# Kernel tuning notes

Hardware: AMD Instinct MI355X
Metric: run time of the kernel (lower is better)

## Reference

```python
import jax, jax.numpy as jnp
import numpy as np

B, T, Z, S, H = 32, 128, 100, 6, 64
F1, F2 = 512, 128


def setup_inputs() -> dict:
    key = jax.random.key(0)
    ks = jax.random.split(key, 11)
    g = lambda k, shape, sc: (jax.random.normal(k, shape, dtype=jnp.float32) * sc)
    return {
        "x": jax.random.normal(ks[0], (B, T, Z, S), dtype=jnp.float32),
        "W_ih": g(ks[1], (3 * H, S), 0.125),   # GRU input weights [r|z|n]
        "W_hh": g(ks[2], (3 * H, H), 0.125),   # GRU hidden weights [r|z|n]
        "b_ih": g(ks[3], (3 * H,), 0.125),
        "b_hh": g(ks[4], (3 * H,), 0.125),
        "w1": g(ks[5], (F1, H), 0.1),
        "b1": g(ks[6], (F1,), 0.1),
        "w2": g(ks[7], (F2, F1), 0.04),
        "b2": g(ks[8], (F2,), 0.04),
        "w3": g(ks[9], (1, F2), 0.09),
        "b3": g(ks[10], (1,), 0.09),
    }


def reference(x, W_ih, W_hh, b_ih, b_hh, w1, b1, w2, b2, w3, b3):
    b, t, z, s = x.shape
    h_dim = W_hh.shape[1]
    # Fuse the per-zone python loop into the batch dim, zone-major so the
    # final reshape matches torch.stack(a).view(-1, t, nzones).
    xm = jnp.transpose(x, (2, 0, 1, 3)).reshape(z * b, t, s)  # (ZB, T, S)
    # Precompute input projections for all timesteps (one big GEMM).
    gi_all = jnp.einsum('nts,gs->ntg', xm, W_ih) + b_ih        # (ZB, T, 3H)

    def step(h, gi):
        gh = h @ W_hh.T + b_hh
        r = jax.nn.sigmoid(gi[:, :h_dim] + gh[:, :h_dim])
        zg = jax.nn.sigmoid(gi[:, h_dim:2 * h_dim] + gh[:, h_dim:2 * h_dim])
        n = jnp.tanh(gi[:, 2 * h_dim:] + r * gh[:, 2 * h_dim:])
        h_new = (1.0 - zg) * n + zg * h
        return h_new, h_new

    h0 = jnp.zeros((z * b, h_dim), x.dtype)
    _, sx = jax.lax.scan(step, h0, jnp.swapaxes(gi_all, 0, 1))  # (T, ZB, H)
    sx = jnp.swapaxes(sx, 0, 1)                                  # (ZB, T, H)

    a1 = jax.nn.relu(sx @ w1.T + b1)
    a2 = jax.nn.relu(a1 @ w2.T + b2)
    a3 = a2 @ w3.T + b3                                          # (ZB, T, 1)
    return a3.reshape(-1, t, z)                                  # (B, T, Z)
```

## Files before the change

### kernel.cpp

```cpp
#include <hip/hip_runtime.h>
#include <stdint.h>

#define Tdim 128
#define Zdim 100
#define Sdim 6
#define Hdim 64
#define ZB   3200
#define F1   512
#define F2   128
#define Mrows (ZB * Tdim)

typedef _Float16 f16x8 __attribute__((ext_vector_type(8)));
typedef _Float16 f16x4 __attribute__((ext_vector_type(4)));
typedef float f32x4 __attribute__((ext_vector_type(4)));
typedef uint32_t u32x4 __attribute__((ext_vector_type(4)));

__device__ __forceinline__ float sigmoidf_fast(float x) {
  return 1.f / (1.f + __expf(-x));
}
__device__ __forceinline__ float tanhf_fast(float x) {
  return 1.f - 2.f / (__expf(2.f * x) + 1.f);
}

__global__ __launch_bounds__(256) void prep_kernel(
    const float* __restrict__ W_ih, const float* __restrict__ W_hh,
    const float* __restrict__ w1, const float* __restrict__ w2,
    _Float16* __restrict__ Wf, _Float16* __restrict__ w1p,
    _Float16* __restrict__ w2p) {
  int i = blockIdx.x * 256 + threadIdx.x;
  if (i < 192 * 96) {
    int g = i / 96, k = i - g * 96;
    float v = (k < 64) ? W_hh[g * 64 + k] : ((k < 70) ? W_ih[g * 6 + (k - 64)] : 0.f);
    Wf[i] = (_Float16)v;
  }
  int j = i - 192 * 96;
  if (j >= 0 && j < 16 * 32 * 72) {
    int kt = j / 2304, r = j - kt * 2304;
    int f1 = r / 72, h = r - f1 * 72;
    w1p[j] = (_Float16)((h < 64) ? w1[(kt * 32 + f1) * 64 + h] : 0.f);
  }
  int l = j - 16 * 32 * 72;
  if (l >= 0 && l < 16 * 128 * 40) {
    int kt = l / 5120, r = l - kt * 5120;
    int f2 = r / 40, k = r - f2 * 40;
    w2p[l] = (_Float16)((k < 32) ? w2[f2 * 512 + kt * 32 + k] : 0.f);
  }
}

__global__ __launch_bounds__(256, 1) void gru_kernel(
    const float* __restrict__ x, const _Float16* __restrict__ Wf,
    const float* __restrict__ b_ih, const float* __restrict__ b_hh,
    _Float16* __restrict__ sx) {
  __shared__ __align__(16) _Float16 hist[32][16][72];
  __shared__ __align__(16) _Float16 xs[Tdim][16][8];
  const int tid = threadIdx.x;
  const int lane = tid & 63;
  const int w = tid >> 6;
  const int c = lane & 15;
  const int q = lane >> 4;

  for (int i = 0; i < 8; i++) {
    int idx = i * 256 + tid;
    int t = idx >> 4, row = idx & 15;
    int nr = blockIdx.x * 16 + row;
    const float* p = x + (size_t)(nr & 31) * (Tdim * Zdim * Sdim)
                       + (size_t)t * (Zdim * Sdim) + (size_t)(nr >> 5) * Sdim;
    f16x8 v;
    v[0] = (_Float16)p[0]; v[1] = (_Float16)p[1]; v[2] = (_Float16)p[2];
    v[3] = (_Float16)p[3]; v[4] = (_Float16)p[4]; v[5] = (_Float16)p[5];
    v[6] = (_Float16)0.f;  v[7] = (_Float16)0.f;
    *(f16x8*)&xs[t][row][0] = v;
  }

  const int gr0 = w * 16;
  const int gz0 = 64 + w * 16;
  const int gn0 = 128 + w * 16;

  f16x8 Ar[3], Az[3], Anh[2], Ani;
#pragma unroll
  for (int kf = 0; kf < 3; kf++) {
    Ar[kf] = *(const f16x8*)(Wf + (size_t)(gr0 + c) * 96 + kf * 32 + q * 8);
    Az[kf] = *(const f16x8*)(Wf + (size_t)(gz0 + c) * 96 + kf * 32 + q * 8);
  }
  Anh[0] = *(const f16x8*)(Wf + (size_t)(gn0 + c) * 96 + q * 8);
  Anh[1] = *(const f16x8*)(Wf + (size_t)(gn0 + c) * 96 + 32 + q * 8);
  Ani    = *(const f16x8*)(Wf + (size_t)(gn0 + c) * 96 + 64 + q * 8);

  f32x4 Cr, Cz, Cnh, Cni;
  {
    f32x4 bir = *(const f32x4*)(b_ih + gr0 + q * 4);
    f32x4 bhr = *(const f32x4*)(b_hh + gr0 + q * 4);
    f32x4 biz = *(const f32x4*)(b_ih + gz0 + q * 4);
    f32x4 bhz = *(const f32x4*)(b_hh + gz0 + q * 4);
#pragma unroll
    for (int r = 0; r < 4; r++) { Cr[r] = bir[r] + bhr[r]; Cz[r] = biz[r] + bhz[r]; }
    Cnh = *(const f32x4*)(b_hh + gn0 + q * 4);
    Cni = *(const f32x4*)(b_ih + gn0 + q * 4);
  }

  __syncthreads();

  f16x8 Bh0 = {0, 0, 0, 0, 0, 0, 0, 0};
  f16x8 Bh1 = {0, 0, 0, 0, 0, 0, 0, 0};
  f32x4 hprev = {0.f, 0.f, 0.f, 0.f};

  for (int t = 0; t < Tdim; t++) {
    const int tc = t & 31;
    f16x8 xv8 = *(const f16x8*)&xs[t][c][0];
    f16x8 Bx;
#pragma unroll
    for (int j = 0; j < 8; j++) Bx[j] = (q == 0) ? xv8[j] : (_Float16)0.f;

    f32x4 Dni = __builtin_amdgcn_mfma_f32_16x16x32_f16(Ani, Bx, Cni, 0, 0, 0);
    f32x4 Dr  = __builtin_amdgcn_mfma_f32_16x16x32_f16(Ar[2], Bx, Cr, 0, 0, 0);
    f32x4 Dz  = __builtin_amdgcn_mfma_f32_16x16x32_f16(Az[2], Bx, Cz, 0, 0, 0);
    f32x4 Dnh = __builtin_amdgcn_mfma_f32_16x16x32_f16(Anh[0], Bh0, Cnh, 0, 0, 0);
    Dr  = __builtin_amdgcn_mfma_f32_16x16x32_f16(Ar[0], Bh0, Dr, 0, 0, 0);
    Dz  = __builtin_amdgcn_mfma_f32_16x16x32_f16(Az[0], Bh0, Dz, 0, 0, 0);
    Dnh = __builtin_amdgcn_mfma_f32_16x16x32_f16(Anh[1], Bh1, Dnh, 0, 0, 0);
    Dr  = __builtin_amdgcn_mfma_f32_16x16x32_f16(Ar[1], Bh1, Dr, 0, 0, 0);
    Dz  = __builtin_amdgcn_mfma_f32_16x16x32_f16(Az[1], Bh1, Dz, 0, 0, 0);

    f16x4 pk;
#pragma unroll
    for (int r = 0; r < 4; r++) {
      float rr = sigmoidf_fast(Dr[r]);
      float zg = sigmoidf_fast(Dz[r]);
      float nn = tanhf_fast(Dni[r] + rr * Dnh[r]);
      float hnew = nn + zg * (hprev[r] - nn);
      hprev[r] = hnew;
      pk[r] = (_Float16)hnew;
    }
    *(f16x4*)&hist[tc][c][w * 16 + q * 4] = pk;
    __syncthreads();
    Bh0 = *(const f16x8*)&hist[tc][c][q * 8];
    Bh1 = *(const f16x8*)&hist[tc][c][32 + q * 8];

    if (tc == 31) {
      const int t0 = t - 31;
#pragma unroll
      for (int rr2 = 0; rr2 < 4; rr2++) {
        const int row = w * 4 + rr2;
        const int nrow = blockIdx.x * 16 + row;
        _Float16* dst = sx + (size_t)nrow * Tdim * Hdim + (size_t)t0 * Hdim;
#pragma unroll
        for (int it = 0; it < 4; it++) {
          int idx = it * 64 + lane;
          int tcc = idx >> 3, hd8 = idx & 7;
          f16x8 vv = *(const f16x8*)&hist[tcc][row][hd8 * 8];
          *(f16x8*)(dst + tcc * 64 + hd8 * 8) = vv;
        }
      }
      __syncthreads();
    }
  }
}

__global__ __launch_bounds__(256, 3) void mlp_kernel(
    const _Float16* __restrict__ sx, const _Float16* __restrict__ w1p,
    const _Float16* __restrict__ w2p, const float* __restrict__ b1,
    const float* __restrict__ b2, const float* __restrict__ w3,
    const float* __restrict__ b3, float* __restrict__ out) {
  __shared__ __align__(16) _Float16 w1s[2][32][72];
  __shared__ __align__(16) _Float16 w2s[2][128][40];
  __shared__ __align__(16) _Float16 rep[4][2][2][16][36];
  const int tid = threadIdx.x;
  const int lane = tid & 63;
  const int wave = tid >> 6;
  const int c = lane & 15;
  const int q = lane >> 4;
  const size_t m0 = ((size_t)blockIdx.x * 4 + wave) * 32;

  f16x8 Bs[2][2];
#pragma unroll
  for (int g = 0; g < 2; g++)
#pragma unroll
    for (int kk = 0; kk < 2; kk++)
      Bs[g][kk] = *(const f16x8*)(sx + (m0 + g * 16 + c) * Hdim + kk * 32 + q * 8);

  f32x4 acc2[2][8];
#pragma unroll
  for (int g = 0; g < 2; g++)
#pragma unroll
    for (int nt = 0; nt < 8; nt++) acc2[g][nt] = (f32x4){0.f, 0.f, 0.f, 0.f};

  u32x4 r1a, r1b, r2a, r2b, r2c;
  {
    const u32x4* g1 = (const u32x4*)(w1p);
    const u32x4* g2 = (const u32x4*)(w2p);
    r1a = g1[tid];
    if (tid < 32) r1b = g1[256 + tid];
    r2a = g2[tid];
    r2b = g2[256 + tid];
    if (tid < 128) r2c = g2[512 + tid];
    u32x4* s1 = (u32x4*)&w1s[0][0][0];
    u32x4* s2 = (u32x4*)&w2s[0][0][0];
    s1[tid] = r1a;
    if (tid < 32) s1[256 + tid] = r1b;
    s2[tid] = r2a;
    s2[256 + tid] = r2b;
    if (tid < 128) s2[512 + tid] = r2c;
  }
  __syncthreads();

#pragma unroll 2
  for (int kt = 0; kt < 16; kt++) {
    const int buf = kt & 1;
    if (kt + 1 < 16) {
      const u32x4* g1 = (const u32x4*)(w1p + (size_t)(kt + 1) * 2304);
      const u32x4* g2 = (const u32x4*)(w2p + (size_t)(kt + 1) * 5120);
      r1a = g1[tid];
      if (tid < 32) r1b = g1[256 + tid];
      r2a = g2[tid];
      r2b = g2[256 + tid];
      if (tid < 128) r2c = g2[512 + tid];
    }

#pragma unroll
    for (int ntl = 0; ntl < 2; ntl++) {
      const int f1b = kt * 32 + ntl * 16;
      f16x8 A0 = *(const f16x8*)&w1s[buf][ntl * 16 + c][q * 8];
      f16x8 A1 = *(const f16x8*)&w1s[buf][ntl * 16 + c][32 + q * 8];
      f32x4 bb = *(const f32x4*)(b1 + f1b + q * 4);
#pragma unroll
      for (int g = 0; g < 2; g++) {
        f32x4 cc = {0.f, 0.f, 0.f, 0.f};
        cc = __builtin_amdgcn_mfma_f32_16x16x32_f16(A0, Bs[g][0], cc, 0, 0, 0);
        cc = __builtin_amdgcn_mfma_f32_16x16x32_f16(A1, Bs[g][1], cc, 0, 0, 0);
        f16x4 pk;
#pragma unroll
        for (int r = 0; r < 4; r++) {
          float v = cc[r] + bb[r];
          pk[r] = (_Float16)(v > 0.f ? v : 0.f);
        }
        *(f16x4*)&rep[wave][buf][g][c][ntl * 16 + q * 4] = pk;
      }
    }
    f16x8 Ba[2];
#pragma unroll
    for (int g = 0; g < 2; g++) {
      f16x4 lo = *(const f16x4*)&rep[wave][buf][g][c][q * 8];
      f16x4 hi = *(const f16x4*)&rep[wave][buf][g][c][q * 8 + 4];
#pragma unroll
      for (int j = 0; j < 4; j++) { Ba[g][j] = lo[j]; Ba[g][4 + j] = hi[j]; }
    }
#pragma unroll
    for (int nt = 0; nt < 8; nt++) {
      f16x8 A2 = *(const f16x8*)&w2s[buf][nt * 16 + c][q * 8];
#pragma unroll
      for (int g = 0; g < 2; g++)
        acc2[g][nt] = __builtin_amdgcn_mfma_f32_16x16x32_f16(A2, Ba[g], acc2[g][nt], 0, 0, 0);
    }

    if (kt + 1 < 16) {
      u32x4* s1 = (u32x4*)&w1s[buf ^ 1][0][0];
      u32x4* s2 = (u32x4*)&w2s[buf ^ 1][0][0];
      s1[tid] = r1a;
      if (tid < 32) s1[256 + tid] = r1b;
      s2[tid] = r2a;
      s2[256 + tid] = r2b;
      if (tid < 128) s2[512 + tid] = r2c;
      __syncthreads();
    }
  }

  float part[2] = {0.f, 0.f};
#pragma unroll
  for (int nt = 0; nt < 8; nt++) {
    f32x4 bb = *(const f32x4*)(b2 + nt * 16 + q * 4);
    f32x4 ww = *(const f32x4*)(w3 + nt * 16 + q * 4);
#pragma unroll
    for (int g = 0; g < 2; g++) {
#pragma unroll
      for (int r = 0; r < 4; r++) {
        float v = acc2[g][nt][r] + bb[r];
        v = v > 0.f ? v : 0.f;
        part[g] = fmaf(v, ww[r], part[g]);
      }
    }
  }
#pragma unroll
  for (int g = 0; g < 2; g++) {
    part[g] += __shfl_xor(part[g], 16, 64);
    part[g] += __shfl_xor(part[g], 32, 64);
  }
  if (q < 2) {
    float pv = (q == 0) ? part[0] : part[1];
    out[m0 + q * 16 + c] = pv + b3[0];
  }
}

extern "C" void kernel_launch(void* const* d_in, const int* in_sizes, int n_in,
                              void* d_out, int out_size, void* d_ws, size_t ws_size,
                              hipStream_t stream) {
  const float* x    = (const float*)d_in[0];
  const float* W_ih = (const float*)d_in[1];
  const float* W_hh = (const float*)d_in[2];
  const float* b_ih = (const float*)d_in[3];
  const float* b_hh = (const float*)d_in[4];
  const float* w1   = (const float*)d_in[5];
  const float* b1   = (const float*)d_in[6];
  const float* w2   = (const float*)d_in[7];
  const float* b2   = (const float*)d_in[8];
  const float* w3   = (const float*)d_in[9];
  const float* b3   = (const float*)d_in[10];
  float* out = (float*)d_out;

  char* ws = (char*)d_ws;
  _Float16* sxf = (_Float16*)ws;
  _Float16* Wf  = (_Float16*)(ws + 52428800);
  _Float16* w1p = (_Float16*)(ws + 52428800 + 36864);
  _Float16* w2p = (_Float16*)(ws + 52428800 + 36864 + 73728);

  hipLaunchKernelGGL(prep_kernel, dim3(536), dim3(256), 0, stream,
                     W_ih, W_hh, w1, w2, Wf, w1p, w2p);
  hipLaunchKernelGGL(gru_kernel, dim3(ZB / 16), dim3(256), 0, stream,
                     x, Wf, b_ih, b_hh, sxf);
  hipLaunchKernelGGL(mlp_kernel, dim3(Mrows / 128), dim3(256), 0, stream,
                     sxf, w1p, w2p, b1, b2, w3, b3, out);
}
```

Before: 260.9 us.

## Pre-swizzle MLP weights into MFMA fragment order and restructure GRU time loop

The prep kernel now writes w1 and w2 in lane-major MFMA fragment order, so the MLP kernel reads each A operand and the relu'd intermediate with one contiguous 16-byte LDS load per lane. This replaces the padded row layouts and the split lo/hi gathers. The padding and the partial-thread copies go away, shrinking LDS and global weight traffic. Separately, the GRU time loop is split into four 32-step chunks with unrolling disabled, removing the per-step branch that flushed history. This risks LDS bank conflicts under the new contiguous layout, and the loop-structure change may alter how instructions are scheduled.

```diff
diff --git a/kernel.cpp b/kernel.cpp
--- a/kernel.cpp
+++ b/kernel.cpp
@@ -34,16 +34,22 @@
     Wf[i] = (_Float16)v;
   }
   int j = i - 192 * 96;
-  if (j >= 0 && j < 16 * 32 * 72) {
-    int kt = j / 2304, r = j - kt * 2304;
-    int f1 = r / 72, h = r - f1 * 72;
-    w1p[j] = (_Float16)((h < 64) ? w1[(kt * 32 + f1) * 64 + h] : 0.f);
-  }
-  int l = j - 16 * 32 * 72;
-  if (l >= 0 && l < 16 * 128 * 40) {
-    int kt = l / 5120, r = l - kt * 5120;
-    int f2 = r / 40, k = r - f2 * 40;
-    w2p[l] = (_Float16)((k < 32) ? w2[f2 * 512 + kt * 32 + k] : 0.f);
+  if (j >= 0 && j < 32768) {
+    int kt = j >> 11, ntl = (j >> 10) & 1, kf = (j >> 9) & 1;
+    int lane = (j >> 3) & 63, e = j & 7;
+    int q = lane >> 4, c = lane & 15;
+    int row = kt * 32 + ntl * 16 + c;
+    int h = kf * 32 + q * 8 + e;
+    w1p[j] = (_Float16)w1[row * 64 + h];
+  }
+  int l = j - 32768;
+  if (l >= 0 && l < 65536) {
+    int kt = l >> 12, nt = (l >> 9) & 7;
+    int lane = (l >> 3) & 63, e = l & 7;
+    int q = lane >> 4, c = lane & 15;
+    int row = nt * 16 + c;
+    int k = kt * 32 + q * 8 + e;
+    w2p[l] = (_Float16)w2[row * 512 + k];
   }
 }
 
@@ -104,40 +110,43 @@
   f16x8 Bh1 = {0, 0, 0, 0, 0, 0, 0, 0};
   f32x4 hprev = {0.f, 0.f, 0.f, 0.f};
 
-  for (int t = 0; t < Tdim; t++) {
-    const int tc = t & 31;
-    f16x8 xv8 = *(const f16x8*)&xs[t][c][0];
-    f16x8 Bx;
-#pragma unroll
-    for (int j = 0; j < 8; j++) Bx[j] = (q == 0) ? xv8[j] : (_Float16)0.f;
-
-    f32x4 Dni = __builtin_amdgcn_mfma_f32_16x16x32_f16(Ani, Bx, Cni, 0, 0, 0);
-    f32x4 Dr  = __builtin_amdgcn_mfma_f32_16x16x32_f16(Ar[2], Bx, Cr, 0, 0, 0);
-    f32x4 Dz  = __builtin_amdgcn_mfma_f32_16x16x32_f16(Az[2], Bx, Cz, 0, 0, 0);
-    f32x4 Dnh = __builtin_amdgcn_mfma_f32_16x16x32_f16(Anh[0], Bh0, Cnh, 0, 0, 0);
-    Dr  = __builtin_amdgcn_mfma_f32_16x16x32_f16(Ar[0], Bh0, Dr, 0, 0, 0);
-    Dz  = __builtin_amdgcn_mfma_f32_16x16x32_f16(Az[0], Bh0, Dz, 0, 0, 0);
-    Dnh = __builtin_amdgcn_mfma_f32_16x16x32_f16(Anh[1], Bh1, Dnh, 0, 0, 0);
-    Dr  = __builtin_amdgcn_mfma_f32_16x16x32_f16(Ar[1], Bh1, Dr, 0, 0, 0);
-    Dz  = __builtin_amdgcn_mfma_f32_16x16x32_f16(Az[1], Bh1, Dz, 0, 0, 0);
-
-    f16x4 pk;
-#pragma unroll
-    for (int r = 0; r < 4; r++) {
-      float rr = sigmoidf_fast(Dr[r]);
-      float zg = sigmoidf_fast(Dz[r]);
-      float nn = tanhf_fast(Dni[r] + rr * Dnh[r]);
-      float hnew = nn + zg * (hprev[r] - nn);
-      hprev[r] = hnew;
-      pk[r] = (_Float16)hnew;
-    }
-    *(f16x4*)&hist[tc][c][w * 16 + q * 4] = pk;
-    __syncthreads();
-    Bh0 = *(const f16x8*)&hist[tc][c][q * 8];
-    Bh1 = *(const f16x8*)&hist[tc][c][32 + q * 8];
-
-    if (tc == 31) {
-      const int t0 = t - 31;
+#pragma unroll 1
+  for (int tch = 0; tch < 4; tch++) {
+#pragma unroll 1
+    for (int tc = 0; tc < 32; tc++) {
+      const int t = tch * 32 + tc;
+      f16x8 xv8 = *(const f16x8*)&xs[t][c][0];
+      f16x8 Bx;
+#pragma unroll
+      for (int j = 0; j < 8; j++) Bx[j] = (q == 0) ? xv8[j] : (_Float16)0.f;
+
+      f32x4 Dni = __builtin_amdgcn_mfma_f32_16x16x32_f16(Ani, Bx, Cni, 0, 0, 0);
+      f32x4 Dr  = __builtin_amdgcn_mfma_f32_16x16x32_f16(Ar[2], Bx, Cr, 0, 0, 0);
+      f32x4 Dz  = __builtin_amdgcn_mfma_f32_16x16x32_f16(Az[2], Bx, Cz, 0, 0, 0);
+      f32x4 Dnh = __builtin_amdgcn_mfma_f32_16x16x32_f16(Anh[0], Bh0, Cnh, 0, 0, 0);
+      Dr  = __builtin_amdgcn_mfma_f32_16x16x32_f16(Ar[0], Bh0, Dr, 0, 0, 0);
+      Dz  = __builtin_amdgcn_mfma_f32_16x16x32_f16(Az[0], Bh0, Dz, 0, 0, 0);
+      Dnh = __builtin_amdgcn_mfma_f32_16x16x32_f16(Anh[1], Bh1, Dnh, 0, 0, 0);
+      Dr  = __builtin_amdgcn_mfma_f32_16x16x32_f16(Ar[1], Bh1, Dr, 0, 0, 0);
+      Dz  = __builtin_amdgcn_mfma_f32_16x16x32_f16(Az[1], Bh1, Dz, 0, 0, 0);
+
+      f16x4 pk;
+#pragma unroll
+      for (int r = 0; r < 4; r++) {
+        float rr = sigmoidf_fast(Dr[r]);
+        float zg = sigmoidf_fast(Dz[r]);
+        float nn = tanhf_fast(Dni[r] + rr * Dnh[r]);
+        float hnew = nn + zg * (hprev[r] - nn);
+        hprev[r] = hnew;
+        pk[r] = (_Float16)hnew;
+      }
+      *(f16x4*)&hist[tc][c][w * 16 + q * 4] = pk;
+      __syncthreads();
+      Bh0 = *(const f16x8*)&hist[tc][c][q * 8];
+      Bh1 = *(const f16x8*)&hist[tc][c][32 + q * 8];
+    }
+    {
+      const int t0 = tch * 32;
 #pragma unroll
       for (int rr2 = 0; rr2 < 4; rr2++) {
         const int row = w * 4 + rr2;
@@ -161,9 +170,9 @@
     const _Float16* __restrict__ w2p, const float* __restrict__ b1,
     const float* __restrict__ b2, const float* __restrict__ w3,
     const float* __restrict__ b3, float* __restrict__ out) {
-  __shared__ __align__(16) _Float16 w1s[2][32][72];
-  __shared__ __align__(16) _Float16 w2s[2][128][40];
-  __shared__ __align__(16) _Float16 rep[4][2][2][16][36];
+  __shared__ __align__(16) _Float16 w1s[2][2048];
+  __shared__ __align__(16) _Float16 w2s[2][4096];
+  __shared__ __align__(16) _Float16 rep[4][2][2][512];
   const int tid = threadIdx.x;
   const int lane = tid & 63;
   const int wave = tid >> 6;
@@ -184,22 +193,16 @@
 #pragma unroll
     for (int nt = 0; nt < 8; nt++) acc2[g][nt] = (f32x4){0.f, 0.f, 0.f, 0.f};
 
-  u32x4 r1a, r1b, r2a, r2b, r2c;
+  u32x4 r1, r2a, r2b;
   {
     const u32x4* g1 = (const u32x4*)(w1p);
     const u32x4* g2 = (const u32x4*)(w2p);
-    r1a = g1[tid];
-    if (tid < 32) r1b = g1[256 + tid];
+    r1 = g1[tid];
     r2a = g2[tid];
     r2b = g2[256 + tid];
-    if (tid < 128) r2c = g2[512 + tid];
-    u32x4* s1 = (u32x4*)&w1s[0][0][0];
-    u32x4* s2 = (u32x4*)&w2s[0][0][0];
-    s1[tid] = r1a;
-    if (tid < 32) s1[256 + tid] = r1b;
-    s2[tid] = r2a;
-    s2[256 + tid] = r2b;
-    if (tid < 128) s2[512 + tid] = r2c;
+    ((u32x4*)&w1s[0][0])[tid] = r1;
+    ((u32x4*)&w2s[0][0])[tid] = r2a;
+    ((u32x4*)&w2s[0][0])[256 + tid] = r2b;
   }
   __syncthreads();
 
@@ -207,21 +210,20 @@
   for (int kt = 0; kt < 16; kt++) {
     const int buf = kt & 1;
     if (kt + 1 < 16) {
-      const u32x4* g1 = (const u32x4*)(w1p + (size_t)(kt + 1) * 2304);
-      const u32x4* g2 = (const u32x4*)(w2p + (size_t)(kt + 1) * 5120);
-      r1a = g1[tid];
-      if (tid < 32) r1b = g1[256 + tid];
+      const u32x4* g1 = (const u32x4*)(w1p + (size_t)(kt + 1) * 2048);
+      const u32x4* g2 = (const u32x4*)(w2p + (size_t)(kt + 1) * 4096);
+      r1 = g1[tid];
       r2a = g2[tid];
       r2b = g2[256 + tid];
-      if (tid < 128) r2c = g2[512 + tid];
     }
 
 #pragma unroll
     for (int ntl = 0; ntl < 2; ntl++) {
       const int f1b = kt * 32 + ntl * 16;
-      f16x8 A0 = *(const f16x8*)&w1s[buf][ntl * 16 + c][q * 8];
-      f16x8 A1 = *(const f16x8*)&w1s[buf][ntl * 16 + c][32 + q * 8];
+      f16x8 A0 = *(const f16x8*)&w1s[buf][ntl * 1024 + lane * 8];
+      f16x8 A1 = *(const f16x8*)&w1s[buf][ntl * 1024 + 512 + lane * 8];
       f32x4 bb = *(const f32x4*)(b1 + f1b + q * 4);
+      const int roff = ((2 * ntl + (q >> 1)) * 16 + c) * 8 + (q & 1) * 4;
 #pragma unroll
       for (int g = 0; g < 2; g++) {
         f32x4 cc = {0.f, 0.f, 0.f, 0.f};
@@ -233,33 +235,25 @@
           float v = cc[r] + bb[r];
           pk[r] = (_Float16)(v > 0.f ? v : 0.f);
         }
-        *(f16x4*)&rep[wave][buf][g][c][ntl * 16 + q * 4] = pk;
+        *(f16x4*)&rep[wave][buf][g][roff] = pk;
       }
     }
     f16x8 Ba[2];
 #pragma unroll
-    for (int g = 0; g < 2; g++) {
-      f16x4 lo = *(const f16x4*)&rep[wave][buf][g][c][q * 8];
-      f16x4 hi = *(const f16x4*)&rep[wave][buf][g][c][q * 8 + 4];
-#pragma unroll
-      for (int j = 0; j < 4; j++) { Ba[g][j] = lo[j]; Ba[g][4 + j] = hi[j]; }
-    }
+    for (int g = 0; g < 2; g++)
+      Ba[g] = *(const f16x8*)&rep[wave][buf][g][lane * 8];
 #pragma unroll
     for (int nt = 0; nt < 8; nt++) {
-      f16x8 A2 = *(const f16x8*)&w2s[buf][nt * 16 + c][q * 8];
+      f16x8 A2 = *(const f16x8*)&w2s[buf][nt * 512 + lane * 8];
 #pragma unroll
       for (int g = 0; g < 2; g++)
         acc2[g][nt] = __builtin_amdgcn_mfma_f32_16x16x32_f16(A2, Ba[g], acc2[g][nt], 0, 0, 0);
     }
 
     if (kt + 1 < 16) {
-      u32x4* s1 = (u32x4*)&w1s[buf ^ 1][0][0];
-      u32x4* s2 = (u32x4*)&w2s[buf ^ 1][0][0];
-      s1[tid] = r1a;
-      if (tid < 32) s1[256 + tid] = r1b;
-      s2[tid] = r2a;
-      s2[256 + tid] = r2b;
-      if (tid < 128) s2[512 + tid] = r2c;
+      ((u32x4*)&w1s[buf ^ 1][0])[tid] = r1;
+      ((u32x4*)&w2s[buf ^ 1][0])[tid] = r2a;
+      ((u32x4*)&w2s[buf ^ 1][0])[256 + tid] = r2b;
       __syncthreads();
     }
   }
@@ -310,9 +304,9 @@
   _Float16* sxf = (_Float16*)ws;
   _Float16* Wf  = (_Float16*)(ws + 52428800);
   _Float16* w1p = (_Float16*)(ws + 52428800 + 36864);
-  _Float16* w2p = (_Float16*)(ws + 52428800 + 36864 + 73728);
-
-  hipLaunchKernelGGL(prep_kernel, dim3(536), dim3(256), 0, stream,
+  _Float16* w2p = (_Float16*)(ws + 52428800 + 36864 + 65536);
+
+  hipLaunchKernelGGL(prep_kernel, dim3(456), dim3(256), 0, stream,
                      W_ih, W_hh, w1, w2, Wf, w1p, w2p);
   hipLaunchKernelGGL(gru_kernel, dim3(ZB / 16), dim3(256), 0, stream,
                      x, Wf, b_ih, b_hh, sxf);
```

After: 257.4 us. About the same (-1.4%).
